# Kernel optimization log

Measured on AMD Instinct MI355X. Metric: run time of the kernel, lower is better.

Reference implementation:

```python
import jax, jax.numpy as jnp
import numpy as np

B, N, D_IN = 2, 2048, 2048
D_OUT, H, KV = 2048, 32, 8
G = H // KV          # group_size = 4
DH = D_OUT // H      # head dim = 64


def setup_inputs() -> dict:
    key = jax.random.key(0)
    k0, k1, k2, k3, k4, k5 = jax.random.split(key, 6)
    s_in = 1.0 / np.sqrt(D_IN)
    s_out = 1.0 / np.sqrt(D_OUT)
    return {
        "x": jax.random.normal(k0, (B, N, D_IN), dtype=jnp.float32),
        "Wq": jax.random.normal(k1, (D_IN, H * DH), dtype=jnp.float32) * s_in,
        "Wk": jax.random.normal(k2, (D_IN, KV * DH), dtype=jnp.float32) * s_in,
        "Wv": jax.random.normal(k3, (D_IN, KV * DH), dtype=jnp.float32) * s_in,
        "Wo": jax.random.normal(k4, (D_OUT, D_IN), dtype=jnp.float32) * s_out,
        "bo": jax.random.normal(k5, (D_IN,), dtype=jnp.float32) * 0.01,
    }


def gqa_forward(x, Wq, Wk, Wv, Wo, bo):
    b, n, _ = x.shape
    scale = 1.0 / jnp.sqrt(jnp.asarray(DH, x.dtype))
    # projections
    q = (x @ Wq).reshape(b, n, KV, G, DH)   # queries grouped by shared kv head
    k = (x @ Wk).reshape(b, n, KV, DH)
    v = (x @ Wv).reshape(b, n, KV, DH)
    # scores: (B, KV, G, N, N) — equivalent to repeat_interleave of K over groups
    scores = jnp.einsum('bnkgd,bmkd->bkgnm', q, k) * scale
    causal = jnp.triu(jnp.ones((n, n), dtype=bool), k=1)
    scores = jnp.where(causal, -jnp.inf, scores)
    attn = jax.nn.softmax(scores, axis=-1)
    # dropout p=0.0 -> identity
    ctx = jnp.einsum('bkgnm,bmkd->bnkgd', attn, v).reshape(b, n, D_OUT)
    return ctx @ Wo + bo


def reference(x, Wq, Wk, Wv, Wo, bo):
    return gqa_forward(x, Wq, Wk, Wv, Wo, bo)
```

## Files before the change

kernel.cpp:

```cpp
#include <hip/hip_runtime.h>
#include <hip/hip_bf16.h>
#include <cstdint>


#define B_    2
#define N_    2048
#define DIN_  2048
#define H_    32
#define KV_   8
#define DH_   64
#define M_    4096
#define NQKV_ 3072

typedef float f32x4 __attribute__((ext_vector_type(4)));
typedef __bf16 bf16x8 __attribute__((ext_vector_type(8)));
typedef unsigned short u16x8 __attribute__((ext_vector_type(8)));

__device__ __forceinline__ unsigned short f32_to_bf16_bits(float f) {
  unsigned int u = __float_as_uint(f);
  u = (u + 0x7FFFu + ((u >> 16) & 1u)) >> 16;
  return (unsigned short)u;
}

__device__ __forceinline__ void gload_lds16(const void* g, void* l) {
  __builtin_amdgcn_global_load_lds(
      (__attribute__((address_space(1))) void*)(g),
      (__attribute__((address_space(3))) void*)(l), 16, 0, 0);
}

__global__ __launch_bounds__(256) void prep(
    const float* __restrict__ x, const float* __restrict__ Wq,
    const float* __restrict__ Wk, const float* __restrict__ Wv,
    const float* __restrict__ Wo,
    unsigned short* __restrict__ Xb, unsigned short* __restrict__ Wqkv,
    unsigned short* __restrict__ Wot, float qscale) {
  const int task = blockIdx.y, tid = threadIdx.x;
  if (task == 0) {
    size_t base = (size_t)blockIdx.x * 1024;
#pragma unroll
    for (int t = 0; t < 4; ++t) {
      size_t i = base + t * 256 + tid;
      float4 v = ((const float4*)x)[i];
      ushort4 o;
      o.x = f32_to_bf16_bits(v.x);
      o.y = f32_to_bf16_bits(v.y);
      o.z = f32_to_bf16_bits(v.z);
      o.w = f32_to_bf16_bits(v.w);
      ((ushort4*)Xb)[i] = o;
    }
    return;
  }
  const float* src;
  unsigned short* dst;
  int NC, off;
  float scale = 1.0f;
  switch (task) {
    case 1: src = Wq; dst = Wqkv; NC = 2048; off = 0;    scale = qscale; break;
    case 2: src = Wk; dst = Wqkv; NC = 512;  off = 2048; break;
    case 3: src = Wv; dst = Wqkv; NC = 512;  off = 2560; break;
    default: src = Wo; dst = Wot; NC = 2048; off = 0;    break;
  }
  const int nbn = NC >> 6;
  if (blockIdx.x >= 32 * nbn) return;
  const int n0 = (blockIdx.x % nbn) * 64, k0 = (blockIdx.x / nbn) * 64;

  __shared__ float tile[64][68];
  const int tx = tid & 15, ty = tid >> 4;
#pragma unroll
  for (int i = 0; i < 4; ++i) {
    float4 v = *(const float4*)&src[(size_t)(k0 + i * 16 + ty) * NC + n0 + tx * 4];
    *(float4*)&tile[i * 16 + ty][tx * 4] = v;
  }
  __syncthreads();
  const int n = tid >> 2, kc = (tid & 3) * 16;
  unsigned short* drow = dst + (size_t)(off + n0 + n) * 2048 + k0 + kc;
#pragma unroll
  for (int h = 0; h < 2; ++h) {
    u16x8 o;
#pragma unroll
    for (int j = 0; j < 8; ++j)
      o[j] = f32_to_bf16_bits(tile[kc + h * 8 + j][n] * scale);
    *(u16x8*)(drow + h * 8) = o;
  }
}

__global__ __launch_bounds__(256) void transpose_v(
    const unsigned short* __restrict__ QKV, unsigned short* __restrict__ Vtg) {
  __shared__ unsigned short t[64][72];
  int nt = blockIdx.x, bkv = blockIdx.y;
  int b = bkv >> 3, kv = bkv & 7;
  int tid = threadIdx.x;
  int row = tid >> 2, c = (tid & 3) * 16;
  const unsigned short* src =
      QKV + (size_t)(b * N_ + nt * 64 + row) * NQKV_ + 2560 + kv * 64;
  *(u16x8*)&t[row][c]     = *(const u16x8*)(src + c);
  *(u16x8*)&t[row][c + 8] = *(const u16x8*)(src + c + 8);
  __syncthreads();
  int d = tid >> 2;
  unsigned short* dst = Vtg + ((size_t)bkv * 64 + d) * N_ + nt * 64 + c;
  u16x8 o0, o1;
#pragma unroll
  for (int i = 0; i < 8; ++i) { o0[i] = t[c + i][d]; o1[i] = t[c + 8 + i][d]; }
  *(u16x8*)dst = o0;
  *(u16x8*)(dst + 8) = o1;
}

template <int BM, int BN, bool OUT_BF16, bool BIAS>
__global__ __launch_bounds__(512, 2) void gemm256p(
    const unsigned short* __restrict__ A,
    const unsigned short* __restrict__ Bt,
    void* __restrict__ Cv,
    const float* __restrict__ bias,
    int Nn, int K, int nbx) {
  constexpr int AL = BM / 64;
  constexpr int BL = BN / 64;
  constexpr int STL = AL + BL;
  constexpr int RM = BM / 2;
  constexpr int CW = BN / 4;
  constexpr int MI = RM / 16;
  constexpr int NI = CW / 16;
  constexpr int NP = MI / 2;

  __shared__ unsigned short ldsA[2][BM * 64];
  __shared__ unsigned short ldsB[2][BN * 64];

  const int tid = threadIdx.x;
  const int lane = tid & 63;
  const int wave = tid >> 6;
  const int wm = wave >> 2, wn = wave & 3;
  const int l16 = lane & 15, quad = lane >> 4;

  const int nwg = gridDim.x;
  const int orig = blockIdx.x;
  const int bid = (orig & 7) * (nwg >> 3) + (orig >> 3);
  const int m0 = (bid / nbx) * BM, n0 = (bid % nbx) * BN;

  const int T = K >> 6;

  auto stage = [&](int c) {
    const int buf = c & 1;
#pragma unroll
    for (int i = 0; i < AL; ++i) {
      int off = i * 8192 + tid * 16;
      int row = off >> 7;
      int kch = ((off >> 4) & 7) ^ (row & 7);
      gload_lds16(A + (size_t)(m0 + row) * K + c * 64 + kch * 8,
                  (char*)&ldsA[buf][0] + off);
    }
#pragma unroll
    for (int i = 0; i < BL; ++i) {
      int off = i * 8192 + tid * 16;
      int row = off >> 7;
      int kch = ((off >> 4) & 7) ^ (row & 7);
      gload_lds16(Bt + (size_t)(n0 + row) * K + c * 64 + kch * 8,
                  (char*)&ldsB[buf][0] + off);
    }
  };

  const int sw7 = l16 & 7;
  const int cA0 = ((0 * 4 + quad) ^ sw7) * 16;
  const int cA1 = ((1 * 4 + quad) ^ sw7) * 16;
  const int rowA = (wm * RM + l16) * 128;
  const int rowB = (wn * CW + l16) * 128;

  f32x4 acc[MI][NI] = {};

  stage(0);
  stage(1);

  for (int c = 0; c < T; ++c) {
    if (c + 1 < T) {
      if constexpr (STL == 6)      asm volatile("s_waitcnt vmcnt(6)" ::: "memory");
      else if constexpr (STL == 7) asm volatile("s_waitcnt vmcnt(7)" ::: "memory");
      else                         asm volatile("s_waitcnt vmcnt(8)" ::: "memory");
    } else {
      asm volatile("s_waitcnt vmcnt(0)" ::: "memory");
    }
    __builtin_amdgcn_s_barrier();
    asm volatile("" ::: "memory");

    const char* Ar = (const char*)&ldsA[c & 1][0];
    const char* Br = (const char*)&ldsB[c & 1][0];

    bf16x8 b[NI][2];
#pragma unroll
    for (int ni = 0; ni < NI; ++ni) {
      b[ni][0] = *(const bf16x8*)(Br + rowB + ni * 2048 + cA0);
      b[ni][1] = *(const bf16x8*)(Br + rowB + ni * 2048 + cA1);
    }
    bf16x8 ap[2][2][2];
#pragma unroll
    for (int ml = 0; ml < 2; ++ml) {
      ap[0][ml][0] = *(const bf16x8*)(Ar + rowA + ml * 2048 + cA0);
      ap[0][ml][1] = *(const bf16x8*)(Ar + rowA + ml * 2048 + cA1);
    }
    asm volatile("s_waitcnt lgkmcnt(0)" ::: "memory");
    __builtin_amdgcn_sched_barrier(0);

#pragma unroll
    for (int p = 0; p < NP; ++p) {
      if (p < NP - 1) {
        const int nx = (p + 1) & 1;
#pragma unroll
        for (int ml = 0; ml < 2; ++ml) {
          int mi = (p + 1) * 2 + ml;
          ap[nx][ml][0] = *(const bf16x8*)(Ar + rowA + mi * 2048 + cA0);
          ap[nx][ml][1] = *(const bf16x8*)(Ar + rowA + mi * 2048 + cA1);
        }
      }
      __builtin_amdgcn_sched_barrier(0);
      __builtin_amdgcn_s_setprio(1);
#pragma unroll
      for (int ml = 0; ml < 2; ++ml)
#pragma unroll
        for (int ni = 0; ni < NI; ++ni)
#pragma unroll
          for (int ks = 0; ks < 2; ++ks)
            acc[p * 2 + ml][ni] = __builtin_amdgcn_mfma_f32_16x16x32_bf16(
                ap[p & 1][ml][ks], b[ni][ks], acc[p * 2 + ml][ni], 0, 0, 0);
      __builtin_amdgcn_s_setprio(0);
      if (p < NP - 1) {
        asm volatile("s_waitcnt lgkmcnt(0)" ::: "memory");
        __builtin_amdgcn_sched_barrier(0);
      }
    }

    asm volatile("" ::: "memory");
    __builtin_amdgcn_s_barrier();
    asm volatile("" ::: "memory");
    if (c + 2 < T) stage(c + 2);
  }

  unsigned short* Cb = (unsigned short*)Cv;
  float* Cf = (float*)Cv;
#pragma unroll
  for (int mi = 0; mi < MI; ++mi) {
    int rrow = m0 + wm * RM + mi * 16 + quad * 4;
#pragma unroll
    for (int ni = 0; ni < NI; ++ni) {
      int col = n0 + wn * CW + ni * 16 + l16;
      float bv = BIAS ? bias[col] : 0.0f;
#pragma unroll
      for (int r = 0; r < 4; ++r) {
        float v = acc[mi][ni][r] + bv;
        if (OUT_BF16)
          Cb[(size_t)(rrow + r) * Nn + col] = f32_to_bf16_bits(v);
        else
          Cf[(size_t)(rrow + r) * Nn + col] = v;
      }
    }
  }
}

__global__ __launch_bounds__(256, 2) void attn_fwd(
    const unsigned short* __restrict__ QKV,
    const unsigned short* __restrict__ Vtg,
    unsigned short* __restrict__ Ctx) {
  __shared__ unsigned short Ks[2][64 * 64];
  __shared__ unsigned short Vs[2][64 * 64];
  __shared__ unsigned short Ps[2][4][2][16 * 64];

  const int p = blockIdx.x;
  const int kv = blockIdx.y >> 1, hp = blockIdx.y & 1;
  const int b = blockIdx.z;
  const int tid = threadIdx.x, lane = tid & 63, wave = tid >> 6;
  const int l16 = lane & 15, quad = lane >> 4;
  const int h = kv * 4 + hp * 2 + (wave >> 1);
  const int rhalf = (wave & 1) * 32;
  const size_t baserow = (size_t)b * N_;
  const unsigned short* Kg = QKV + 2048 + kv * 64;
  const unsigned short* Vg = Vtg + (size_t)(b * KV_ + kv) * 64 * N_;
  const unsigned short* Qbase = QKV + baserow * NQKV_ + h * 64;
  const int sw = l16 & 7;

  auto stageKV = [&](int j, int buf) {
#pragma unroll
    for (int it = 0; it < 2; ++it) {
      int c = tid + it * 256;
      int row = c >> 3, off = ((c & 7) ^ (row & 7)) * 8;
      gload_lds16(Kg + (baserow + j * 64 + row) * NQKV_ + off,
                  (char*)Ks[buf] + c * 16);
      gload_lds16(Vg + (size_t)row * N_ + j * 64 + off,
                  (char*)Vs[buf] + c * 16);
    }
  };

#pragma unroll 1
  for (int phase = 0; phase < 2; ++phase) {
    const int qtile = phase ? p : 31 - p;
    const int q0 = qtile * 64;

    bf16x8 qa[2][2];
#pragma unroll
    for (int s = 0; s < 2; ++s)
#pragma unroll
      for (int ks = 0; ks < 2; ++ks)
        qa[s][ks] = *(const bf16x8*)(Qbase +
            (size_t)(q0 + rhalf + s * 16 + l16) * NQKV_ + ks * 32 + quad * 8);

    f32x4 oacc[2][4] = {};
    float lp[2][4] = {};

    __syncthreads();
    stageKV(0, 0);

    for (int j = 0; j <= qtile; ++j) {
      __syncthreads();
      const int buf = j & 1;
      if (j < qtile) stageKV(j + 1, buf ^ 1);

      bf16x8 kb[2][4];
#pragma unroll
      for (int ks = 0; ks < 2; ++ks)
#pragma unroll
        for (int ni = 0; ni < 4; ++ni)
          kb[ks][ni] = *(const bf16x8*)&Ks[buf][(ni * 16 + l16) * 64 +
                                               ((ks * 4 + quad) ^ sw) * 8];

#pragma unroll
      for (int s = 0; s < 2; ++s) {
        f32x4 sc[4] = {};
        __builtin_amdgcn_s_setprio(1);
#pragma unroll
        for (int ks = 0; ks < 2; ++ks)
#pragma unroll
          for (int ni = 0; ni < 4; ++ni)
            sc[ni] = __builtin_amdgcn_mfma_f32_16x16x32_bf16(
                qa[s][ks], kb[ks][ni], sc[ni], 0, 0, 0);
        __builtin_amdgcn_s_setprio(0);
        if (j == qtile) {
          const int qrow = q0 + rhalf + s * 16 + quad * 4;
#pragma unroll
          for (int ni = 0; ni < 4; ++ni) {
            int kcol = q0 + ni * 16 + l16;
#pragma unroll
            for (int r = 0; r < 4; ++r)
              if (kcol > qrow + r) sc[ni][r] = -1e30f;
          }
        }
        unsigned short* Pw = &Ps[buf][wave][s][0];
#pragma unroll
        for (int ni = 0; ni < 4; ++ni) {
          const int cl = ni * 2 + (l16 >> 3);
#pragma unroll
          for (int r = 0; r < 4; ++r) {
            float pe = __builtin_amdgcn_exp2f(sc[ni][r]);
            lp[s][r] += pe;
            int row = quad * 4 + r;
            Pw[row * 64 + ((cl ^ (row & 7)) * 8) + (l16 & 7)] =
                (unsigned short)(__float_as_uint(pe) >> 16);
          }
        }
      }

      bf16x8 vb[2][4];
#pragma unroll
      for (int ks = 0; ks < 2; ++ks)
#pragma unroll
        for (int di = 0; di < 4; ++di)
          vb[ks][di] = *(const bf16x8*)&Vs[buf][(di * 16 + l16) * 64 +
                                               ((ks * 4 + quad) ^ sw) * 8];
#pragma unroll
      for (int s = 0; s < 2; ++s) {
        bf16x8 pa[2];
#pragma unroll
        for (int ks = 0; ks < 2; ++ks)
          pa[ks] = *(const bf16x8*)&Ps[buf][wave][s][l16 * 64 +
                                                    ((ks * 4 + quad) ^ sw) * 8];
        __builtin_amdgcn_s_setprio(1);
#pragma unroll
        for (int ks = 0; ks < 2; ++ks)
#pragma unroll
          for (int di = 0; di < 4; ++di)
            oacc[s][di] = __builtin_amdgcn_mfma_f32_16x16x32_bf16(
                pa[ks], vb[ks][di], oacc[s][di], 0, 0, 0);
        __builtin_amdgcn_s_setprio(0);
      }
    }

#pragma unroll
    for (int s = 0; s < 2; ++s) {
      float inv[4];
#pragma unroll
      for (int r = 0; r < 4; ++r) {
        float v = lp[s][r];
#pragma unroll
        for (int off = 1; off < 16; off <<= 1) v += __shfl_xor(v, off);
        inv[r] = 1.0f / v;
      }
#pragma unroll
      for (int di = 0; di < 4; ++di)
#pragma unroll
        for (int r = 0; r < 4; ++r) {
          size_t row = baserow + q0 + rhalf + s * 16 + quad * 4 + r;
          Ctx[row * 2048 + h * 64 + di * 16 + l16] =
              f32_to_bf16_bits(oacc[s][di][r] * inv[r]);
        }
    }
  }
}

extern "C" void kernel_launch(void* const* d_in, const int* in_sizes, int n_in,
                              void* d_out, int out_size, void* d_ws, size_t ws_size,
                              hipStream_t stream) {
  const float* x  = (const float*)d_in[0];
  const float* Wq = (const float*)d_in[1];
  const float* Wk = (const float*)d_in[2];
  const float* Wv = (const float*)d_in[3];
  const float* Wo = (const float*)d_in[4];
  const float* bo = (const float*)d_in[5];
  float* out = (float*)d_out;

  unsigned short* Xb   = (unsigned short*)d_ws;
  unsigned short* Wqkv = Xb + (size_t)M_ * DIN_;
  unsigned short* QKV  = Wqkv + (size_t)NQKV_ * DIN_;
  unsigned short* Wot  = QKV + (size_t)M_ * NQKV_;
  unsigned short* Ctx  = Xb;
  unsigned short* Vtg  = Wqkv;

  const float kQScale = 0.125f * 1.44269504088896340736f;

  prep<<<dim3(2048, 5), 256, 0, stream>>>(x, Wq, Wk, Wv, Wo, Xb, Wqkv, Wot, kQScale);

  gemm256p<256, 192, true, false><<<dim3(256), 512, 0, stream>>>(
      Xb, Wqkv, QKV, nullptr, NQKV_, DIN_, NQKV_ / 192);

  transpose_v<<<dim3(N_ / 64, B_ * KV_), 256, 0, stream>>>(QKV, Vtg);

  attn_fwd<<<dim3(16, 16, 2), 256, 0, stream>>>(QKV, Vtg, Ctx);

  gemm256p<128, 256, false, true><<<dim3(256), 512, 0, stream>>>(
      Ctx, Wot, out, bo, DIN_, 2048, DIN_ / 256);
}
```

Baseline: 280.6 us.

## Split attention work across 8 waves with one 16-row strip each

The attention kernel now launches 512 threads per block, so each wave handles a single 16-row query strip for one head instead of two strips. Per-wave registers for Q fragments, accumulators and row sums are halved, and KV staging drops to one load per thread. The aim is more waves in flight per CU to hide latency. In exchange, every wave still reloads the full K and V fragments from LDS for only half the MFMA work, which doubles LDS read traffic per FLOP and puts more waves behind each barrier.

```diff
diff --git a/kernel.cpp b/kernel.cpp
--- a/kernel.cpp
+++ b/kernel.cpp
@@ -252,21 +252,21 @@
   }
 }
 
-__global__ __launch_bounds__(256, 2) void attn_fwd(
+__global__ __launch_bounds__(512, 4) void attn_fwd(
     const unsigned short* __restrict__ QKV,
     const unsigned short* __restrict__ Vtg,
     unsigned short* __restrict__ Ctx) {
   __shared__ unsigned short Ks[2][64 * 64];
   __shared__ unsigned short Vs[2][64 * 64];
-  __shared__ unsigned short Ps[2][4][2][16 * 64];
+  __shared__ unsigned short Ps[2][8][16 * 64];
 
   const int p = blockIdx.x;
   const int kv = blockIdx.y >> 1, hp = blockIdx.y & 1;
   const int b = blockIdx.z;
   const int tid = threadIdx.x, lane = tid & 63, wave = tid >> 6;
   const int l16 = lane & 15, quad = lane >> 4;
-  const int h = kv * 4 + hp * 2 + (wave >> 1);
-  const int rhalf = (wave & 1) * 32;
+  const int h = kv * 4 + hp * 2 + (wave >> 2);
+  const int rstrip = (wave & 3) * 16;
   const size_t baserow = (size_t)b * N_;
   const unsigned short* Kg = QKV + 2048 + kv * 64;
   const unsigned short* Vg = Vtg + (size_t)(b * KV_ + kv) * 64 * N_;
@@ -274,15 +274,12 @@
   const int sw = l16 & 7;
 
   auto stageKV = [&](int j, int buf) {
-#pragma unroll
-    for (int it = 0; it < 2; ++it) {
-      int c = tid + it * 256;
-      int row = c >> 3, off = ((c & 7) ^ (row & 7)) * 8;
-      gload_lds16(Kg + (baserow + j * 64 + row) * NQKV_ + off,
-                  (char*)Ks[buf] + c * 16);
-      gload_lds16(Vg + (size_t)row * N_ + j * 64 + off,
-                  (char*)Vs[buf] + c * 16);
-    }
+    int c = tid;
+    int row = c >> 3, off = ((c & 7) ^ (row & 7)) * 8;
+    gload_lds16(Kg + (baserow + j * 64 + row) * NQKV_ + off,
+                (char*)Ks[buf] + c * 16);
+    gload_lds16(Vg + (size_t)row * N_ + j * 64 + off,
+                (char*)Vs[buf] + c * 16);
   };
 
 #pragma unroll 1
@@ -290,16 +287,14 @@
     const int qtile = phase ? p : 31 - p;
     const int q0 = qtile * 64;
 
-    bf16x8 qa[2][2];
-#pragma unroll
-    for (int s = 0; s < 2; ++s)
-#pragma unroll
-      for (int ks = 0; ks < 2; ++ks)
-        qa[s][ks] = *(const bf16x8*)(Qbase +
-            (size_t)(q0 + rhalf + s * 16 + l16) * NQKV_ + ks * 32 + quad * 8);
-
-    f32x4 oacc[2][4] = {};
-    float lp[2][4] = {};
+    bf16x8 qa[2];
+#pragma unroll
+    for (int ks = 0; ks < 2; ++ks)
+      qa[ks] = *(const bf16x8*)(Qbase +
+          (size_t)(q0 + rstrip + l16) * NQKV_ + ks * 32 + quad * 8);
+
+    f32x4 oacc[4] = {};
+    float lp[4] = {};
 
     __syncthreads();
     stageKV(0, 0);
@@ -317,39 +312,36 @@
           kb[ks][ni] = *(const bf16x8*)&Ks[buf][(ni * 16 + l16) * 64 +
                                                ((ks * 4 + quad) ^ sw) * 8];
 
-#pragma unroll
-      for (int s = 0; s < 2; ++s) {
-        f32x4 sc[4] = {};
-        __builtin_amdgcn_s_setprio(1);
-#pragma unroll
-        for (int ks = 0; ks < 2; ++ks)
-#pragma unroll
-          for (int ni = 0; ni < 4; ++ni)
-            sc[ni] = __builtin_amdgcn_mfma_f32_16x16x32_bf16(
-                qa[s][ks], kb[ks][ni], sc[ni], 0, 0, 0);
-        __builtin_amdgcn_s_setprio(0);
-        if (j == qtile) {
-          const int qrow = q0 + rhalf + s * 16 + quad * 4;
-#pragma unroll
-          for (int ni = 0; ni < 4; ++ni) {
-            int kcol = q0 + ni * 16 + l16;
-#pragma unroll
-            for (int r = 0; r < 4; ++r)
-              if (kcol > qrow + r) sc[ni][r] = -1e30f;
-          }
+      f32x4 sc[4] = {};
+      __builtin_amdgcn_s_setprio(1);
+#pragma unroll
+      for (int ks = 0; ks < 2; ++ks)
+#pragma unroll
+        for (int ni = 0; ni < 4; ++ni)
+          sc[ni] = __builtin_amdgcn_mfma_f32_16x16x32_bf16(
+              qa[ks], kb[ks][ni], sc[ni], 0, 0, 0);
+      __builtin_amdgcn_s_setprio(0);
+      if (j == qtile) {
+        const int qrow = q0 + rstrip + quad * 4;
+#pragma unroll
+        for (int ni = 0; ni < 4; ++ni) {
+          int kcol = q0 + ni * 16 + l16;
+#pragma unroll
+          for (int r = 0; r < 4; ++r)
+            if (kcol > qrow + r) sc[ni][r] = -1e30f;
         }
-        unsigned short* Pw = &Ps[buf][wave][s][0];
-#pragma unroll
-        for (int ni = 0; ni < 4; ++ni) {
-          const int cl = ni * 2 + (l16 >> 3);
-#pragma unroll
-          for (int r = 0; r < 4; ++r) {
-            float pe = __builtin_amdgcn_exp2f(sc[ni][r]);
-            lp[s][r] += pe;
-            int row = quad * 4 + r;
-            Pw[row * 64 + ((cl ^ (row & 7)) * 8) + (l16 & 7)] =
-                (unsigned short)(__float_as_uint(pe) >> 16);
-          }
+      }
+      unsigned short* Pw = &Ps[buf][wave][0];
+#pragma unroll
+      for (int ni = 0; ni < 4; ++ni) {
+        const int cl = ni * 2 + (l16 >> 3);
+#pragma unroll
+        for (int r = 0; r < 4; ++r) {
+          float pe = __builtin_amdgcn_exp2f(sc[ni][r]);
+          lp[r] += pe;
+          int row = quad * 4 + r;
+          Pw[row * 64 + ((cl ^ (row & 7)) * 8) + (l16 & 7)] =
+              (unsigned short)(__float_as_uint(pe) >> 16);
         }
       }
 
@@ -360,43 +352,37 @@
         for (int di = 0; di < 4; ++di)
           vb[ks][di] = *(const bf16x8*)&Vs[buf][(di * 16 + l16) * 64 +
                                                ((ks * 4 + quad) ^ sw) * 8];
-#pragma unroll
-      for (int s = 0; s < 2; ++s) {
-        bf16x8 pa[2];
-#pragma unroll
-        for (int ks = 0; ks < 2; ++ks)
-          pa[ks] = *(const bf16x8*)&Ps[buf][wave][s][l16 * 64 +
-                                                    ((ks * 4 + quad) ^ sw) * 8];
-        __builtin_amdgcn_s_setprio(1);
-#pragma unroll
-        for (int ks = 0; ks < 2; ++ks)
-#pragma unroll
-          for (int di = 0; di < 4; ++di)
-            oacc[s][di] = __builtin_amdgcn_mfma_f32_16x16x32_bf16(
-                pa[ks], vb[ks][di], oacc[s][di], 0, 0, 0);
-        __builtin_amdgcn_s_setprio(0);
-      }
-    }
-
-#pragma unroll
-    for (int s = 0; s < 2; ++s) {
-      float inv[4];
+      bf16x8 pa[2];
+#pragma unroll
+      for (int ks = 0; ks < 2; ++ks)
+        pa[ks] = *(const bf16x8*)&Ps[buf][wave][l16 * 64 +
+                                               ((ks * 4 + quad) ^ sw) * 8];
+      __builtin_amdgcn_s_setprio(1);
+#pragma unroll
+      for (int ks = 0; ks < 2; ++ks)
+#pragma unroll
+        for (int di = 0; di < 4; ++di)
+          oacc[di] = __builtin_amdgcn_mfma_f32_16x16x32_bf16(
+              pa[ks], vb[ks][di], oacc[di], 0, 0, 0);
+      __builtin_amdgcn_s_setprio(0);
+    }
+
+    float inv[4];
+#pragma unroll
+    for (int r = 0; r < 4; ++r) {
+      float v = lp[r];
+#pragma unroll
+      for (int off = 1; off < 16; off <<= 1) v += __shfl_xor(v, off);
+      inv[r] = 1.0f / v;
+    }
+#pragma unroll
+    for (int di = 0; di < 4; ++di)
 #pragma unroll
       for (int r = 0; r < 4; ++r) {
-        float v = lp[s][r];
-#pragma unroll
-        for (int off = 1; off < 16; off <<= 1) v += __shfl_xor(v, off);
-        inv[r] = 1.0f / v;
-      }
-#pragma unroll
-      for (int di = 0; di < 4; ++di)
-#pragma unroll
-        for (int r = 0; r < 4; ++r) {
-          size_t row = baserow + q0 + rhalf + s * 16 + quad * 4 + r;
-          Ctx[row * 2048 + h * 64 + di * 16 + l16] =
-              f32_to_bf16_bits(oacc[s][di][r] * inv[r]);
-        }
-    }
+        size_t row = baserow + q0 + rstrip + quad * 4 + r;
+        Ctx[row * 2048 + h * 64 + di * 16 + l16] =
+            f32_to_bf16_bits(oacc[di][r] * inv[r]);
+      }
   }
 }
 
@@ -427,7 +413,7 @@
 
   transpose_v<<<dim3(N_ / 64, B_ * KV_), 256, 0, stream>>>(QKV, Vtg);
 
-  attn_fwd<<<dim3(16, 16, 2), 256, 0, stream>>>(QKV, Vtg, Ctx);
+  attn_fwd<<<dim3(16, 16, 2), 512, 0, stream>>>(QKV, Vtg, Ctx);
 
   gemm256p<128, 256, false, true><<<dim3(256), 512, 0, stream>>>(
       Ctx, Wot, out, bo, DIN_, 2048, DIN_ / 256);
```

Result: no change. 279.7 us (-0.3%).
